# Kernel optimization log

Hardware: AMD Instinct MI355X
Metric: run time of the kernel (lower is better)

## Reference

```python
import jax, jax.numpy as jnp
import numpy as np
import math

N_ENT = 200000
N_USERS = 100000
N_FACTORS = 4
N_REL = 26
CH = 64
N_EDGES = 1000000
NNZ = 1000000
KG_HEADS = 2


def scatter_softmax(scores, seg, num_segments):
    # numerically-stable softmax over groups defined by seg (per-head softmax)
    m = jax.ops.segment_max(scores, seg, num_segments=num_segments)
    m = jnp.where(jnp.isfinite(m), m, 0.0)
    e = jnp.exp(scores - m[seg])
    d = jax.ops.segment_sum(e, seg, num_segments=num_segments)
    return e / d[seg]


def setup_inputs() -> dict:
    key = jax.random.key(0)
    ks = jax.random.split(key, 11)
    return {
        "entity_emb": jax.random.normal(ks[0], (N_ENT, CH), dtype=jnp.float32) * 0.1,
        "user_emb": jax.random.normal(ks[1], (N_USERS, CH), dtype=jnp.float32) * 0.1,
        "latent_emb": jax.random.normal(ks[2], (N_FACTORS, CH), dtype=jnp.float32) * 0.1,
        "edge_index": jax.random.randint(ks[3], (2, N_EDGES), 0, N_ENT),
        "edge_type": jax.random.randint(ks[4], (N_EDGES,), 1, N_REL),  # in [1, N_REL-1]
        "ui_rows": jax.random.randint(ks[5], (NNZ,), 0, N_USERS),
        "ui_cols": jax.random.randint(ks[6], (NNZ,), 0, N_ENT),
        "ui_vals": jax.random.uniform(ks[7], (NNZ,), dtype=jnp.float32),
        "weight": jax.random.normal(ks[8], (N_REL - 1, CH), dtype=jnp.float32) * 0.1,
        "disen_weight_att": jax.random.normal(ks[9], (N_FACTORS, N_REL - 1), dtype=jnp.float32) * 0.1,
        "kg_W_r": jax.random.normal(ks[10], (CH, CH), dtype=jnp.float32) * (1.0 / math.sqrt(CH)),
    }


def reference(entity_emb, user_emb, latent_emb, edge_index, edge_type,
              ui_rows, ui_cols, ui_vals, weight, disen_weight_att, kg_W_r):
    head, tail = edge_index[0], edge_index[1]
    d_k = CH // KG_HEADS

    # --- Invariant_Capture.relation_aware_att ---
    rel_emb = weight[edge_type - 1]            # [E, C] gather
    h_emb = entity_emb[head]                   # [E, C] gather
    q = (h_emb @ kg_W_r).reshape(-1, KG_HEADS, d_k)
    k = (rel_emb @ kg_W_r).reshape(-1, KG_HEADS, d_k)
    score_r = ((q * k).sum(-1) / math.sqrt(d_k)).mean(-1)   # [E]
    rel_attn = scatter_softmax(score_r, head, N_ENT)

    # --- Invariant_Capture.kg_inv_capture ---
    t_emb = entity_emb[tail]                   # [E, C] gather
    r_emb = rel_emb * rel_attn[:, None]
    # bmm(cat(h,r), cat(t,r)^T) == h.t + r.r per edge
    score_trip = (h_emb * t_emb).sum(-1) + (r_emb * r_emb).sum(-1)
    kg_mask = scatter_softmax(score_trip, head, N_ENT)       # invariant_mask [E]

    # --- Aggregator: KG scatter-mean with invariant mask ---
    neigh = t_emb * rel_emb * kg_mask[:, None]               # [E, C]
    sums = jax.ops.segment_sum(neigh, head, num_segments=N_ENT)
    cnt = jax.ops.segment_sum(jnp.ones((neigh.shape[0],), dtype=neigh.dtype), head, num_segments=N_ENT)
    entity_agg = sums / jnp.maximum(cnt, 1.0)[:, None]       # scatter_mean

    # --- Aggregator: user side ---
    score = jax.nn.softmax(user_emb @ latent_emb.T, axis=1)  # [U, F]
    user_agg = jax.ops.segment_sum(entity_emb[ui_cols] * ui_vals[:, None], ui_rows, num_segments=N_USERS)
    disen_weight = jax.nn.softmax(disen_weight_att, axis=-1) @ weight  # [F, C]
    # (expand(U,F,C) * score[:,:,None]).sum(1) == score @ disen_weight
    user_agg = user_agg * (score @ disen_weight) + user_agg

    return jnp.concatenate([entity_agg, user_agg], axis=0)   # [N_ENT+N_USERS, C]
```

## Files before the change

### kernel.cpp

```cpp
#include <hip/hip_runtime.h>
#include <math.h>

#define N_ENT 200000
#define N_USERS 100000
#define NKEY 300000
#define N_FACTORS 4
#define NREL1 25
#define CH 64
#define N_EDGES 1000000
#define NNZ 1000000
#define NREC 2000000
#define BSHIFT 11
#define BKEYS 2048
#define NBUCKET 147
#define TILE 2048
#define CAP 24576

#define SCORE_SCALE 0.08838834764831845f
#define INV_Q14 6.103888176768602e-05f

__device__ __forceinline__ float red8(float d) {
    d += __shfl_xor(d, 1);
    d += __shfl_xor(d, 2);
    d += __shfl_xor(d, 4);
    return d;
}
__device__ __forceinline__ float dot4(float4 a, float4 b) {
    return a.x * b.x + a.y * b.y + a.z * b.z + a.w * b.w;
}
__device__ __forceinline__ unsigned short f2bf(float f) {
    unsigned u = __float_as_uint(f);
    u += 0x7FFFu + ((u >> 16) & 1u);
    return (unsigned short)(u >> 16);
}
__device__ __forceinline__ float bf2f(unsigned short u) {
    return __uint_as_float(((unsigned)u) << 16);
}
__device__ __forceinline__ float4 bf4lo(uint4 t) {
    return make_float4(__uint_as_float(t.x << 16), __uint_as_float(t.x & 0xFFFF0000u),
                       __uint_as_float(t.y << 16), __uint_as_float(t.y & 0xFFFF0000u));
}
__device__ __forceinline__ float4 bf4hi(uint4 t) {
    return make_float4(__uint_as_float(t.z << 16), __uint_as_float(t.z & 0xFFFF0000u),
                       __uint_as_float(t.w << 16), __uint_as_float(t.w & 0xFFFF0000u));
}

__global__ void precompute_k(const float* __restrict__ W,
                             const float* __restrict__ weight,
                             const float* __restrict__ datt,
                             float* __restrict__ Mvec,
                             float* __restrict__ wnorm,
                             float* __restrict__ disen) {
    __shared__ float sW[64 * 64];
    __shared__ float sw[NREL1 * 64];
    __shared__ float sWWt[64 * 64];
    int tid = threadIdx.x;
    for (int i = tid; i < 64 * 64; i += 256) sW[i] = W[i];
    for (int i = tid; i < NREL1 * 64; i += 256) sw[i] = weight[i];
    __syncthreads();
    for (int e = tid; e < 64 * 64; e += 256) {
        int i = e >> 6, j = e & 63;
        float s = 0.f;
        for (int k = 0; k < 64; ++k) s += sW[i * 64 + k] * sW[j * 64 + k];
        sWWt[e] = s;
    }
    __syncthreads();
    for (int e = tid; e < NREL1 * 64; e += 256) {
        int r = e >> 6, i = e & 63;
        float s = 0.f;
        for (int j = 0; j < 64; ++j) s += sWWt[i * 64 + j] * sw[r * 64 + j];
        Mvec[e] = s;
    }
    for (int r = tid; r < NREL1; r += 256) {
        float s = 0.f;
        for (int j = 0; j < 64; ++j) { float v = sw[r * 64 + j]; s += v * v; }
        wnorm[r] = s;
    }
    for (int e = tid; e < N_FACTORS * 64; e += 256) {
        int f = e >> 6, c = e & 63;
        float m = -1e30f;
        for (int r = 0; r < NREL1; ++r) m = fmaxf(m, datt[f * NREL1 + r]);
        float ssum = 0.f, acc = 0.f;
        for (int r = 0; r < NREL1; ++r) {
            float p = expf(datt[f * NREL1 + r] - m);
            ssum += p;
            acc += p * sw[r * 64 + c];
        }
        disen[e] = acc / ssum;
    }
}

__global__ void gcur_init2_k(unsigned* __restrict__ gcur) {
    int b = threadIdx.x;
    if (b < NBUCKET) gcur[b] = (unsigned)b * CAP;
}

__global__ void binfill_k(const int* __restrict__ head, const int* __restrict__ tail,
                          const int* __restrict__ etype,
                          const int* __restrict__ rows, const int* __restrict__ cols,
                          const float* __restrict__ vals,
                          unsigned* __restrict__ gcur,
                          uint2* __restrict__ stg) {
    __shared__ unsigned hist[NBUCKET], base[NBUCKET], gbase[NBUCKET];
    __shared__ unsigned sh[256];
    __shared__ uint2 lrec[TILE];
    int tid = threadIdx.x;
    int tile0 = blockIdx.x * TILE;
    int tile_n = min(TILE, NREC - tile0);
    for (int b = tid; b < NBUCKET; b += 256) hist[b] = 0u;
    __syncthreads();
    unsigned key[8], pay[8], rank[8];
    for (int r = 0; r < 8; ++r) {
        int li = r * 256 + tid;
        key[r] = 0xFFFFFFFFu;
        if (li < tile_n) {
            int idx = tile0 + li;
            unsigned k, p;
            if (idx < N_EDGES) {
                k = (unsigned)head[idx];
                p = (unsigned)tail[idx] | ((unsigned)(etype[idx] - 1) << 18);
            } else {
                int j = idx - N_EDGES;
                k = (unsigned)(N_ENT + rows[j]);
                unsigned q = (unsigned)(vals[j] * 16383.f + 0.5f);
                p = (unsigned)cols[j] | (q << 18);
            }
            key[r] = k; pay[r] = p;
            rank[r] = atomicAdd(&hist[k >> BSHIFT], 1u);
        }
    }
    __syncthreads();
    unsigned v = (tid < NBUCKET) ? hist[tid] : 0u;
    sh[tid] = v; __syncthreads();
    for (int o = 1; o < 256; o <<= 1) {
        unsigned t = (tid >= o) ? sh[tid - o] : 0u;
        __syncthreads();
        sh[tid] += t;
        __syncthreads();
    }
    if (tid < NBUCKET) {
        base[tid] = sh[tid] - v;
        gbase[tid] = v ? atomicAdd(&gcur[tid], v) : 0u;
    }
    __syncthreads();
    for (int r = 0; r < 8; ++r) {
        if (key[r] != 0xFFFFFFFFu) {
            unsigned b = key[r] >> BSHIFT;
            unsigned pos = base[b] + rank[r];
            lrec[pos] = make_uint2(key[r], pay[r]);
        }
    }
    __syncthreads();
    for (int i = tid; i < tile_n; i += 256) {
        uint2 rec = lrec[i];
        unsigned b = rec.x >> BSHIFT;
        unsigned dst = gbase[b] + ((unsigned)i - base[b]);
        if (dst < (b + 1u) * CAP) stg[dst] = rec;
    }
}

__global__ void bucket_scan_k(const unsigned* __restrict__ gcur,
                              unsigned* __restrict__ bbase,
                              unsigned* __restrict__ offs) {
    __shared__ unsigned s[256];
    int tid = threadIdx.x;
    unsigned c = (tid < NBUCKET) ? (gcur[tid] - (unsigned)tid * CAP) : 0u;
    if (c > CAP) c = CAP;
    unsigned v = c;
    s[tid] = v; __syncthreads();
    for (int o = 1; o < 256; o <<= 1) {
        unsigned t = (tid >= o) ? s[tid - o] : 0u;
        __syncthreads();
        s[tid] += t;
        __syncthreads();
    }
    if (tid < NBUCKET) bbase[tid] = s[tid] - v;
    if (tid == 0) offs[NKEY] = NREC;
}

__global__ void binplace2_k(const uint2* __restrict__ stg,
                            const unsigned* __restrict__ gcur,
                            const unsigned* __restrict__ bbase,
                            unsigned* __restrict__ offs,
                            unsigned* __restrict__ csr) {
    __shared__ unsigned cnt[BKEYS];
    __shared__ unsigned sc[1024];
    int b = blockIdx.x;
    int tid = threadIdx.x;
    unsigned n = gcur[b] - (unsigned)b * CAP;
    if (n > CAP) n = CAP;
    unsigned gb = bbase[b];
    const uint2* seg = stg + (size_t)b * CAP;
    cnt[tid * 2] = 0u; cnt[tid * 2 + 1] = 0u;
    __syncthreads();
    for (unsigned i = tid; i < n; i += 1024) {
        unsigned kk = seg[i].x - ((unsigned)b << BSHIFT);
        atomicAdd(&cnt[kk], 1u);
    }
    __syncthreads();
    unsigned c0 = cnt[tid * 2], c1 = cnt[tid * 2 + 1];
    unsigned tsum = c0 + c1;
    sc[tid] = tsum; __syncthreads();
    for (int o = 1; o < 1024; o <<= 1) {
        unsigned t = (tid >= o) ? sc[tid - o] : 0u;
        __syncthreads();
        sc[tid] += t;
        __syncthreads();
    }
    unsigned e0 = sc[tid] - tsum;
    unsigned e1 = e0 + c0;
    int k0 = (b << BSHIFT) + tid * 2;
    if (k0 < NKEY)     offs[k0]     = gb + e0;
    if (k0 + 1 < NKEY) offs[k0 + 1] = gb + e1;
    cnt[tid * 2] = e0; cnt[tid * 2 + 1] = e1;
    __syncthreads();
    for (unsigned i = tid; i < n; i += 1024) {
        uint2 rec = seg[i];
        unsigned kk = rec.x - ((unsigned)b << BSHIFT);
        unsigned pos = atomicAdd(&cnt[kk], 1u);
        csr[gb + pos] = rec.y;
    }
}

__global__ void convE_k(const float* __restrict__ ent,
                        const float* __restrict__ Mvec,
                        uint4* __restrict__ entb,
                        unsigned short* __restrict__ E16) {
    __shared__ float4 sM[NREL1 * 16];
    int tid = threadIdx.x;
    for (int i = tid; i < NREL1 * 16; i += 256) sM[i] = ((const float4*)Mvec)[i];
    __syncthreads();
    int gid = blockIdx.x * 256 + tid;
    int h = gid >> 3;
    int sub = tid & 7;
    if (h >= N_ENT) return;
    const float4* e4 = (const float4*)ent;
    float4 a = e4[h * 16 + sub * 2], b4 = e4[h * 16 + sub * 2 + 1];
    uint4 o;
    o.x = (unsigned)f2bf(a.x)  | ((unsigned)f2bf(a.y)  << 16);
    o.y = (unsigned)f2bf(a.z)  | ((unsigned)f2bf(a.w)  << 16);
    o.z = (unsigned)f2bf(b4.x) | ((unsigned)f2bf(b4.y) << 16);
    o.w = (unsigned)f2bf(b4.z) | ((unsigned)f2bf(b4.w) << 16);
    entb[h * 8 + sub] = o;
    for (int r = 0; r < NREL1; ++r) {
        float d = dot4(a, sM[r * 16 + sub * 2]) + dot4(b4, sM[r * 16 + sub * 2 + 1]);
        d = red8(d);
        if (sub == (r & 7)) E16[h * NREL1 + r] = f2bf(__expf(d * SCORE_SCALE));
    }
}

template<bool FAST>
__global__ void gather8_k(const float* __restrict__ ent,
                          const uint4* __restrict__ entb,
                          const unsigned short* __restrict__ E16,
                          const float* __restrict__ weight,
                          const float* __restrict__ Mvec,
                          const float* __restrict__ wnorm,
                          const float* __restrict__ uemb,
                          const float* __restrict__ lat,
                          const float* __restrict__ disen,
                          const unsigned* __restrict__ offs,
                          const unsigned* __restrict__ csr,
                          float* __restrict__ out) {
    int gid = blockIdx.x * 256 + threadIdx.x;
    int key = gid >> 3;
    int sub = threadIdx.x & 7;
    if (key >= NKEY) return;
    unsigned beg = offs[key], end = offs[key + 1];
    const float4* e4 = (const float4*)ent;
    const float4* w4 = (const float4*)weight;
    float4* o4 = (float4*)out;
    const float4 z = make_float4(0.f, 0.f, 0.f, 0.f);

    if (key < N_ENT) {
        int h = key;
        if (beg == end) {
            o4[h * 16 + sub * 2] = z;
            o4[h * 16 + sub * 2 + 1] = z;
            return;
        }
        float4 hv0 = e4[h * 16 + sub * 2], hv1 = e4[h * 16 + sub * 2 + 1];
        float dr = 0.f;
        if (FAST) {
            for (unsigned i = beg + sub; i < end; i += 8)
                dr += bf2f(E16[h * NREL1 + (csr[i] >> 18)]);
            dr = red8(dr);
        } else {
            for (unsigned i = beg; i < end; ++i) {
                int r = csr[i] >> 18;
                float d = dot4(hv0, ((const float4*)Mvec)[r * 16 + sub * 2]) +
                          dot4(hv1, ((const float4*)Mvec)[r * 16 + sub * 2 + 1]);
                dr += __expf(red8(d) * SCORE_SCALE);
            }
        }
        float inv_dr = 1.0f / dr;
        float4 a0 = z, a1 = z;
        float dt = 0.f;
        unsigned i = beg;
        for (; i + 2 <= end; i += 2) {
            unsigned p0 = csr[i], p1 = csr[i + 1];
            int t0 = p0 & 0x3FFFF, r0 = p0 >> 18;
            int t1 = p1 & 0x3FFFF, r1 = p1 >> 18;
            float4 tv00, tv01, tv10, tv11;
            if (FAST) {
                uint4 tb0 = entb[t0 * 8 + sub];
                uint4 tb1 = entb[t1 * 8 + sub];
                tv00 = bf4lo(tb0); tv01 = bf4hi(tb0);
                tv10 = bf4lo(tb1); tv11 = bf4hi(tb1);
            } else {
                tv00 = e4[t0 * 16 + sub * 2]; tv01 = e4[t0 * 16 + sub * 2 + 1];
                tv10 = e4[t1 * 16 + sub * 2]; tv11 = e4[t1 * 16 + sub * 2 + 1];
            }
            float d0 = red8(dot4(hv0, tv00) + dot4(hv1, tv01));
            float d1 = red8(dot4(hv0, tv10) + dot4(hv1, tv11));
            float er0, er1;
            if (FAST) {
                er0 = bf2f(E16[h * NREL1 + r0]);
                er1 = bf2f(E16[h * NREL1 + r1]);
            } else {
                float q0 = dot4(hv0, ((const float4*)Mvec)[r0 * 16 + sub * 2]) +
                           dot4(hv1, ((const float4*)Mvec)[r0 * 16 + sub * 2 + 1]);
                float q1 = dot4(hv0, ((const float4*)Mvec)[r1 * 16 + sub * 2]) +
                           dot4(hv1, ((const float4*)Mvec)[r1 * 16 + sub * 2 + 1]);
                er0 = __expf(red8(q0) * SCORE_SCALE);
                er1 = __expf(red8(q1) * SCORE_SCALE);
            }
            float ra0 = er0 * inv_dr, ra1 = er1 * inv_dr;
            float et0 = __expf(d0 + ra0 * ra0 * wnorm[r0]);
            float et1 = __expf(d1 + ra1 * ra1 * wnorm[r1]);
            dt += et0 + et1;
            float4 wv;
            wv = w4[r0 * 16 + sub * 2];
            a0.x += et0 * tv00.x * wv.x; a0.y += et0 * tv00.y * wv.y;
            a0.z += et0 * tv00.z * wv.z; a0.w += et0 * tv00.w * wv.w;
            wv = w4[r0 * 16 + sub * 2 + 1];
            a1.x += et0 * tv01.x * wv.x; a1.y += et0 * tv01.y * wv.y;
            a1.z += et0 * tv01.z * wv.z; a1.w += et0 * tv01.w * wv.w;
            wv = w4[r1 * 16 + sub * 2];
            a0.x += et1 * tv10.x * wv.x; a0.y += et1 * tv10.y * wv.y;
            a0.z += et1 * tv10.z * wv.z; a0.w += et1 * tv10.w * wv.w;
            wv = w4[r1 * 16 + sub * 2 + 1];
            a1.x += et1 * tv11.x * wv.x; a1.y += et1 * tv11.y * wv.y;
            a1.z += et1 * tv11.z * wv.z; a1.w += et1 * tv11.w * wv.w;
        }
        if (i < end) {
            unsigned p = csr[i];
            int t = p & 0x3FFFF, r = p >> 18;
            float4 tv0, tv1;
            if (FAST) {
                uint4 tb = entb[t * 8 + sub];
                tv0 = bf4lo(tb); tv1 = bf4hi(tb);
            } else {
                tv0 = e4[t * 16 + sub * 2]; tv1 = e4[t * 16 + sub * 2 + 1];
            }
            float d = red8(dot4(hv0, tv0) + dot4(hv1, tv1));
            float er;
            if (FAST) {
                er = bf2f(E16[h * NREL1 + r]);
            } else {
                float q = dot4(hv0, ((const float4*)Mvec)[r * 16 + sub * 2]) +
                          dot4(hv1, ((const float4*)Mvec)[r * 16 + sub * 2 + 1]);
                er = __expf(red8(q) * SCORE_SCALE);
            }
            float ra = er * inv_dr;
            float et = __expf(d + ra * ra * wnorm[r]);
            dt += et;
            float4 wv;
            wv = w4[r * 16 + sub * 2];
            a0.x += et * tv0.x * wv.x; a0.y += et * tv0.y * wv.y;
            a0.z += et * tv0.z * wv.z; a0.w += et * tv0.w * wv.w;
            wv = w4[r * 16 + sub * 2 + 1];
            a1.x += et * tv1.x * wv.x; a1.y += et * tv1.y * wv.y;
            a1.z += et * tv1.z * wv.z; a1.w += et * tv1.w * wv.w;
        }
        float inv = 1.0f / (dt * (float)(end - beg));
        a0.x *= inv; a0.y *= inv; a0.z *= inv; a0.w *= inv;
        a1.x *= inv; a1.y *= inv; a1.z *= inv; a1.w *= inv;
        o4[h * 16 + sub * 2] = a0;
        o4[h * 16 + sub * 2 + 1] = a1;
    } else {
        int u = key - N_ENT;
        float4 a0 = z, a1 = z;
        unsigned i = beg;
        for (; i + 2 <= end; i += 2) {
            unsigned p0 = csr[i], p1 = csr[i + 1];
            int c0 = p0 & 0x3FFFF, c1 = p1 & 0x3FFFF;
            float v0 = (float)(p0 >> 18) * INV_Q14;
            float v1 = (float)(p1 >> 18) * INV_Q14;
            float4 tv00, tv01, tv10, tv11;
            if (FAST) {
                uint4 tb0 = entb[c0 * 8 + sub];
                uint4 tb1 = entb[c1 * 8 + sub];
                tv00 = bf4lo(tb0); tv01 = bf4hi(tb0);
                tv10 = bf4lo(tb1); tv11 = bf4hi(tb1);
            } else {
                tv00 = e4[c0 * 16 + sub * 2]; tv01 = e4[c0 * 16 + sub * 2 + 1];
                tv10 = e4[c1 * 16 + sub * 2]; tv11 = e4[c1 * 16 + sub * 2 + 1];
            }
            a0.x += v0 * tv00.x + v1 * tv10.x; a0.y += v0 * tv00.y + v1 * tv10.y;
            a0.z += v0 * tv00.z + v1 * tv10.z; a0.w += v0 * tv00.w + v1 * tv10.w;
            a1.x += v0 * tv01.x + v1 * tv11.x; a1.y += v0 * tv01.y + v1 * tv11.y;
            a1.z += v0 * tv01.z + v1 * tv11.z; a1.w += v0 * tv01.w + v1 * tv11.w;
        }
        if (i < end) {
            unsigned p = csr[i];
            int c = p & 0x3FFFF;
            float v = (float)(p >> 18) * INV_Q14;
            float4 tv0, tv1;
            if (FAST) {
                uint4 tb = entb[c * 8 + sub];
                tv0 = bf4lo(tb); tv1 = bf4hi(tb);
            } else {
                tv0 = e4[c * 16 + sub * 2]; tv1 = e4[c * 16 + sub * 2 + 1];
            }
            a0.x += v * tv0.x; a0.y += v * tv0.y; a0.z += v * tv0.z; a0.w += v * tv0.w;
            a1.x += v * tv1.x; a1.y += v * tv1.y; a1.z += v * tv1.z; a1.w += v * tv1.w;
        }
        float4 uv0 = ((const float4*)uemb)[u * 16 + sub * 2];
        float4 uv1 = ((const float4*)uemb)[u * 16 + sub * 2 + 1];
        float d[N_FACTORS];
        for (int f = 0; f < N_FACTORS; ++f) {
            float t = dot4(uv0, ((const float4*)lat)[f * 16 + sub * 2]) +
                      dot4(uv1, ((const float4*)lat)[f * 16 + sub * 2 + 1]);
            d[f] = red8(t);
        }
        float m = fmaxf(fmaxf(d[0], d[1]), fmaxf(d[2], d[3]));
        float s = 0.f, p_[N_FACTORS];
        for (int f = 0; f < N_FACTORS; ++f) { p_[f] = __expf(d[f] - m); s += p_[f]; }
        float invs = 1.0f / s;
        float4 g0 = z, g1 = z;
        for (int f = 0; f < N_FACTORS; ++f) {
            float w = p_[f] * invs;
            float4 dv = ((const float4*)disen)[f * 16 + sub * 2];
            g0.x += w * dv.x; g0.y += w * dv.y; g0.z += w * dv.z; g0.w += w * dv.w;
            dv = ((const float4*)disen)[f * 16 + sub * 2 + 1];
            g1.x += w * dv.x; g1.y += w * dv.y; g1.z += w * dv.z; g1.w += w * dv.w;
        }
        a0.x *= (1.0f + g0.x); a0.y *= (1.0f + g0.y);
        a0.z *= (1.0f + g0.z); a0.w *= (1.0f + g0.w);
        a1.x *= (1.0f + g1.x); a1.y *= (1.0f + g1.y);
        a1.z *= (1.0f + g1.z); a1.w *= (1.0f + g1.w);
        o4[key * 16 + sub * 2] = a0;
        o4[key * 16 + sub * 2 + 1] = a1;
    }
}

extern "C" void kernel_launch(void* const* d_in, const int* in_sizes, int n_in,
                              void* d_out, int out_size, void* d_ws, size_t ws_size,
                              hipStream_t stream) {
    (void)in_sizes; (void)n_in; (void)out_size;
    const float* ent    = (const float*)d_in[0];
    const float* uemb   = (const float*)d_in[1];
    const float* lat    = (const float*)d_in[2];
    const int*   eidx   = (const int*)d_in[3];
    const int*   etype  = (const int*)d_in[4];
    const int*   urows  = (const int*)d_in[5];
    const int*   ucols  = (const int*)d_in[6];
    const float* uvals  = (const float*)d_in[7];
    const float* weight = (const float*)d_in[8];
    const float* datt   = (const float*)d_in[9];
    const float* W      = (const float*)d_in[10];

    const int* head = eidx;
    const int* tail = eidx + N_EDGES;
    float* out = (float*)d_out;

    unsigned* gcur  = (unsigned*)d_ws;
    unsigned* bbase = gcur + 256;
    unsigned* offs  = bbase + 256;
    float*    Mvec  = (float*)(offs + NKEY + 2);
    float*    wnorm = Mvec + NREL1 * 64;
    float*    disen = wnorm + 32;
    unsigned* csr   = (unsigned*)(disen + N_FACTORS * 64);
    unsigned* big   = csr + NREC;
    uint2*    stg   = (uint2*)big;
    unsigned* entb  = big;
    unsigned short* E16 = (unsigned short*)(entb + (size_t)N_ENT * 32);

    size_t base_words = 256 + 256 + (NKEY + 2) + 1888 + (size_t)NREC;
    size_t stg_words  = (size_t)NBUCKET * CAP * 2;
    size_t tbl_words  = (size_t)N_ENT * 32 + ((size_t)N_ENT * NREL1 + 1) / 2;
    size_t big_words  = stg_words > tbl_words ? stg_words : tbl_words;
    size_t need_fast  = (base_words + big_words) * 4;
    size_t need_min   = (base_words + stg_words) * 4;
    bool fast = ws_size >= need_fast;
    if (ws_size < need_min) return;

    const int BLK = 256;

    gcur_init2_k<<<1, 256, 0, stream>>>(gcur);
    precompute_k<<<1, 256, 0, stream>>>(W, weight, datt, Mvec, wnorm, disen);
    binfill_k<<<(NREC + TILE - 1) / TILE, BLK, 0, stream>>>(
        head, tail, etype, urows, ucols, uvals, gcur, stg);
    bucket_scan_k<<<1, 256, 0, stream>>>(gcur, bbase, offs);
    binplace2_k<<<NBUCKET, 1024, 0, stream>>>(stg, gcur, bbase, offs, csr);

    int gridG = (NKEY * 8 + BLK - 1) / BLK;
    if (fast) {
        convE_k<<<(N_ENT * 8 + BLK - 1) / BLK, BLK, 0, stream>>>(
            ent, Mvec, (uint4*)entb, E16);
        gather8_k<true><<<gridG, BLK, 0, stream>>>(
            ent, (const uint4*)entb, E16, weight, Mvec, wnorm,
            uemb, lat, disen, offs, csr, out);
    } else {
        gather8_k<false><<<gridG, BLK, 0, stream>>>(
            ent, (const uint4*)entb, E16, weight, Mvec, wnorm,
            uemb, lat, disen, offs, csr, out);
    }
}
```

Baseline: 224.5 us.

## Fuse bucket scan into bin placement and co-schedule entity conversion

Removes the separate gcur init and bucket-scan kernels. The gcur counters now start at zero via a memset, and every placement block recomputes the bucket prefix scan itself. When the workspace is large enough to hold the staging area and the bf16 tables side by side, bin placement and entity conversion run in one combined launch with heterogeneous blocks, so the conversion work overlaps the placement. This cuts launch count and serial dependencies. The cost is a redundant scan in each of the 147 placement blocks, and conversion blocks now use 1024 threads, which may change occupancy.

```diff
diff --git a/kernel.cpp b/kernel.cpp
--- a/kernel.cpp
+++ b/kernel.cpp
@@ -15,6 +15,7 @@
 #define NBUCKET 147
 #define TILE 2048
 #define CAP 24576
+#define NCONVB ((N_ENT * 8 + 1023) / 1024)
 
 #define SCORE_SCALE 0.08838834764831845f
 #define INV_Q14 6.103888176768602e-05f
@@ -88,11 +89,6 @@
         }
         disen[e] = acc / ssum;
     }
-}
-
-__global__ void gcur_init2_k(unsigned* __restrict__ gcur) {
-    int b = threadIdx.x;
-    if (b < NBUCKET) gcur[b] = (unsigned)b * CAP;
 }
 
 __global__ void binfill_k(const int* __restrict__ head, const int* __restrict__ tail,
@@ -140,7 +136,7 @@
     }
     if (tid < NBUCKET) {
         base[tid] = sh[tid] - v;
-        gbase[tid] = v ? atomicAdd(&gcur[tid], v) : 0u;
+        gbase[tid] = (unsigned)tid * CAP + (v ? atomicAdd(&gcur[tid], v) : 0u);
     }
     __syncthreads();
     for (int r = 0; r < 8; ++r) {
@@ -159,38 +155,32 @@
     }
 }
 
-__global__ void bucket_scan_k(const unsigned* __restrict__ gcur,
-                              unsigned* __restrict__ bbase,
-                              unsigned* __restrict__ offs) {
-    __shared__ unsigned s[256];
-    int tid = threadIdx.x;
-    unsigned c = (tid < NBUCKET) ? (gcur[tid] - (unsigned)tid * CAP) : 0u;
+__device__ __forceinline__
+void place_bucket_dev(int b, int tid, const uint2* __restrict__ stg,
+                      const unsigned* __restrict__ gcur,
+                      unsigned* __restrict__ offs, unsigned* __restrict__ csr,
+                      unsigned* shm) {
+    unsigned c = (tid < NBUCKET) ? gcur[tid] : 0u;
     if (c > CAP) c = CAP;
-    unsigned v = c;
-    s[tid] = v; __syncthreads();
+    if (tid < 256) shm[tid] = c;
+    __syncthreads();
     for (int o = 1; o < 256; o <<= 1) {
-        unsigned t = (tid >= o) ? s[tid - o] : 0u;
+        unsigned t = (tid >= o && tid < 256) ? shm[tid - o] : 0u;
         __syncthreads();
-        s[tid] += t;
+        if (tid < 256) shm[tid] += t;
         __syncthreads();
     }
-    if (tid < NBUCKET) bbase[tid] = s[tid] - v;
-    if (tid == 0) offs[NKEY] = NREC;
-}
-
-__global__ void binplace2_k(const uint2* __restrict__ stg,
-                            const unsigned* __restrict__ gcur,
-                            const unsigned* __restrict__ bbase,
-                            unsigned* __restrict__ offs,
-                            unsigned* __restrict__ csr) {
-    __shared__ unsigned cnt[BKEYS];
-    __shared__ unsigned sc[1024];
-    int b = blockIdx.x;
-    int tid = threadIdx.x;
-    unsigned n = gcur[b] - (unsigned)b * CAP;
-    if (n > CAP) n = CAP;
-    unsigned gb = bbase[b];
+    if (tid == 0) {
+        unsigned cb = gcur[b]; if (cb > CAP) cb = CAP;
+        shm[3073] = cb;
+        shm[3072] = shm[b] - cb;
+        if (b == NBUCKET - 1) offs[NKEY] = shm[NBUCKET - 1];
+    }
+    __syncthreads();
+    unsigned n = shm[3073], gb = shm[3072];
     const uint2* seg = stg + (size_t)b * CAP;
+    unsigned* cnt = shm;
+    unsigned* sc  = shm + 2048;
     cnt[tid * 2] = 0u; cnt[tid * 2 + 1] = 0u;
     __syncthreads();
     for (unsigned i = tid; i < n; i += 1024) {
@@ -222,16 +212,16 @@
     }
 }
 
-__global__ void convE_k(const float* __restrict__ ent,
-                        const float* __restrict__ Mvec,
-                        uint4* __restrict__ entb,
-                        unsigned short* __restrict__ E16) {
-    __shared__ float4 sM[NREL1 * 16];
-    int tid = threadIdx.x;
-    for (int i = tid; i < NREL1 * 16; i += 256) sM[i] = ((const float4*)Mvec)[i];
-    __syncthreads();
-    int gid = blockIdx.x * 256 + tid;
-    int h = gid >> 3;
+__device__ __forceinline__
+void convE_dev(int cb, int tid, const float* __restrict__ ent,
+               const float* __restrict__ Mvec,
+               uint4* __restrict__ entb, unsigned short* __restrict__ E16,
+               unsigned* shm) {
+    float4* sM = (float4*)shm;
+    for (int i = tid; i < NREL1 * 16; i += 1024) sM[i] = ((const float4*)Mvec)[i];
+    __syncthreads();
+    int idx = cb * 1024 + tid;
+    int h = idx >> 3;
     int sub = tid & 7;
     if (h >= N_ENT) return;
     const float4* e4 = (const float4*)ent;
@@ -247,6 +237,38 @@
         d = red8(d);
         if (sub == (r & 7)) E16[h * NREL1 + r] = f2bf(__expf(d * SCORE_SCALE));
     }
+}
+
+__global__ void binplace3_k(const uint2* __restrict__ stg,
+                            const unsigned* __restrict__ gcur,
+                            unsigned* __restrict__ offs,
+                            unsigned* __restrict__ csr) {
+    __shared__ __align__(16) unsigned shm[3074];
+    place_bucket_dev(blockIdx.x, threadIdx.x, stg, gcur, offs, csr, shm);
+}
+
+__global__ void convE2_k(const float* __restrict__ ent,
+                         const float* __restrict__ Mvec,
+                         uint4* __restrict__ entb,
+                         unsigned short* __restrict__ E16) {
+    __shared__ __align__(16) unsigned shm[3074];
+    convE_dev(blockIdx.x, threadIdx.x, ent, Mvec, entb, E16, shm);
+}
+
+__global__ void placeconv_k(const uint2* __restrict__ stg,
+                            const unsigned* __restrict__ gcur,
+                            unsigned* __restrict__ offs,
+                            unsigned* __restrict__ csr,
+                            const float* __restrict__ ent,
+                            const float* __restrict__ Mvec,
+                            uint4* __restrict__ entb,
+                            unsigned short* __restrict__ E16) {
+    __shared__ __align__(16) unsigned shm[3074];
+    int b = blockIdx.x;
+    if (b < NBUCKET)
+        place_bucket_dev(b, threadIdx.x, stg, gcur, offs, csr, shm);
+    else
+        convE_dev(b - NBUCKET, threadIdx.x, ent, Mvec, entb, E16, shm);
 }
 
 template<bool FAST>
@@ -466,45 +488,53 @@
     float* out = (float*)d_out;
 
     unsigned* gcur  = (unsigned*)d_ws;
-    unsigned* bbase = gcur + 256;
-    unsigned* offs  = bbase + 256;
+    unsigned* offs  = gcur + 256;
     float*    Mvec  = (float*)(offs + NKEY + 2);
     float*    wnorm = Mvec + NREL1 * 64;
     float*    disen = wnorm + 32;
     unsigned* csr   = (unsigned*)(disen + N_FACTORS * 64);
     unsigned* big   = csr + NREC;
-    uint2*    stg   = (uint2*)big;
-    unsigned* entb  = big;
-    unsigned short* E16 = (unsigned short*)(entb + (size_t)N_ENT * 32);
-
-    size_t base_words = 256 + 256 + (NKEY + 2) + 1888 + (size_t)NREC;
+
+    size_t base_words = 256 + (NKEY + 2) + 1888 + (size_t)NREC;
     size_t stg_words  = (size_t)NBUCKET * CAP * 2;
     size_t tbl_words  = (size_t)N_ENT * 32 + ((size_t)N_ENT * NREL1 + 1) / 2;
-    size_t big_words  = stg_words > tbl_words ? stg_words : tbl_words;
-    size_t need_fast  = (base_words + big_words) * 4;
-    size_t need_min   = (base_words + stg_words) * 4;
-    bool fast = ws_size >= need_fast;
+    size_t big_alias  = stg_words > tbl_words ? stg_words : tbl_words;
+    size_t need_fast     = (base_words + big_alias) * 4;
+    size_t need_min      = (base_words + stg_words) * 4;
+    size_t need_disjoint = (base_words + stg_words + tbl_words) * 4;
+    bool fast     = ws_size >= need_fast;
+    bool disjoint = ws_size >= need_disjoint;
     if (ws_size < need_min) return;
 
+    uint2*    stg  = (uint2*)big;
+    unsigned* entw = disjoint ? (big + stg_words) : big;
+    uint4*    entb = (uint4*)entw;
+    unsigned short* E16 = (unsigned short*)(entw + (size_t)N_ENT * 32);
+
     const int BLK = 256;
 
-    gcur_init2_k<<<1, 256, 0, stream>>>(gcur);
+    hipMemsetAsync(gcur, 0, 256 * sizeof(unsigned), stream);
     precompute_k<<<1, 256, 0, stream>>>(W, weight, datt, Mvec, wnorm, disen);
     binfill_k<<<(NREC + TILE - 1) / TILE, BLK, 0, stream>>>(
         head, tail, etype, urows, ucols, uvals, gcur, stg);
-    bucket_scan_k<<<1, 256, 0, stream>>>(gcur, bbase, offs);
-    binplace2_k<<<NBUCKET, 1024, 0, stream>>>(stg, gcur, bbase, offs, csr);
+
+    if (disjoint) {
+        placeconv_k<<<NBUCKET + NCONVB, 1024, 0, stream>>>(
+            stg, gcur, offs, csr, ent, Mvec, entb, E16);
+    } else {
+        binplace3_k<<<NBUCKET, 1024, 0, stream>>>(stg, gcur, offs, csr);
+        if (fast)
+            convE2_k<<<NCONVB, 1024, 0, stream>>>(ent, Mvec, entb, E16);
+    }
 
     int gridG = (NKEY * 8 + BLK - 1) / BLK;
     if (fast) {
-        convE_k<<<(N_ENT * 8 + BLK - 1) / BLK, BLK, 0, stream>>>(
-            ent, Mvec, (uint4*)entb, E16);
         gather8_k<true><<<gridG, BLK, 0, stream>>>(
-            ent, (const uint4*)entb, E16, weight, Mvec, wnorm,
+            ent, entb, E16, weight, Mvec, wnorm,
             uemb, lat, disen, offs, csr, out);
     } else {
         gather8_k<false><<<gridG, BLK, 0, stream>>>(
-            ent, (const uint4*)entb, E16, weight, Mvec, wnorm,
+            ent, entb, E16, weight, Mvec, wnorm,
             uemb, lat, disen, offs, csr, out);
     }
 }
```

After: 203.7 us. 1.1x faster.
